# Performance work log

Hardware: AMD Instinct MI355X
Metric: run time of the kernel (lower is better)

The kernel has to match this reference:

```python
import jax, jax.numpy as jnp
import numpy as np

D_MODEL = 1024
NUM_HEADS = 16
KEY_DIM = 64
VALUE_DIM = 64
NEG_INF = jnp.float32(-1e30)


def setup_inputs() -> dict:
    key = jax.random.key(0)
    ks = jax.random.split(key, 10)
    B, S = 2, 2048
    lim = 1.0 / np.sqrt(D_MODEL)
    x = jax.random.normal(ks[0], (B, S, D_MODEL), dtype=jnp.float32)
    mask = jnp.ones((B, S), dtype=jnp.int32)  # pad mask: 1 = keep
    # stacked per-head linear params (Linear stores weight as [out, in])
    Wq = jax.random.uniform(ks[1], (NUM_HEADS, KEY_DIM, D_MODEL), jnp.float32, -lim, lim)
    bq = jax.random.uniform(ks[2], (NUM_HEADS, KEY_DIM), jnp.float32, -lim, lim)
    Wk = jax.random.uniform(ks[3], (NUM_HEADS, KEY_DIM, D_MODEL), jnp.float32, -lim, lim)
    bk = jax.random.uniform(ks[4], (NUM_HEADS, KEY_DIM), jnp.float32, -lim, lim)
    Wv = jax.random.uniform(ks[5], (NUM_HEADS, VALUE_DIM, D_MODEL), jnp.float32, -lim, lim)
    bv = jax.random.uniform(ks[6], (NUM_HEADS, VALUE_DIM), jnp.float32, -lim, lim)
    lim_o = 1.0 / np.sqrt(NUM_HEADS * VALUE_DIM)
    Wo = jax.random.uniform(ks[7], (D_MODEL, NUM_HEADS * VALUE_DIM), jnp.float32, -lim_o, lim_o)
    bo = jax.random.uniform(ks[8], (D_MODEL,), jnp.float32, -lim_o, lim_o)
    return {"x": x, "mask": mask, "Wq": Wq, "bq": bq, "Wk": Wk, "bk": bk,
            "Wv": Wv, "bv": bv, "Wo": Wo, "bo": bo}


def _mha(x, mask, Wq, bq, Wk, bk, Wv, bv, Wo, bo):
    B, S, _ = x.shape
    # per-head projections: [B, H, S, k]
    q = jnp.einsum('bsd,hkd->bhsk', x, Wq) + bq[None, :, None, :]
    k = jnp.einsum('bsd,hkd->bhsk', x, Wk) + bk[None, :, None, :]
    v = jnp.einsum('bsd,hvd->bhsv', x, Wv) + bv[None, :, None, :]
    scale = 1.0 / np.sqrt(KEY_DIM).astype(np.float32)
    scores = jnp.einsum('bhik,bhjk->bhij', q, k) * scale  # [B, H, S, S]
    # final mask = causal AND pad-row AND pad-col
    causal = jnp.tril(jnp.ones((S, S), dtype=bool))
    pad = mask.astype(bool)
    final = causal[None, None] & pad[:, None, :, None] & pad[:, None, None, :]
    masked = jnp.where(final, scores, NEG_INF)
    w = jax.nn.softmax(masked, axis=-1)
    w = jnp.where(final, w, 0.0)  # fully-masked rows -> zeros, matching loop impl
    out = jnp.einsum('bhij,bhjv->bhiv', w, v)            # [B, H, S, V]
    concat = out.transpose(0, 2, 1, 3).reshape(B, S, NUM_HEADS * VALUE_DIM)
    return concat @ Wo.T + bo


def reference(x, mask, Wq, bq, Wk, bk, Wv, bv, Wo, bo):
    return _mha(x, mask, Wq, bq, Wk, bk, Wv, bv, Wo, bo)
```

## Files before the change

kernel.cpp:

```cpp
#include <hip/hip_runtime.h>

#define SEQ 2048
#define NH 16
#define HD 64
#define DMODEL 1024

__device__ __forceinline__ unsigned int f2bf(float f) {
  unsigned int u = __float_as_uint(f);
  return ((u + 0x7fffu + ((u >> 16) & 1u)) >> 16) & 0xffffu;
}

__device__ __forceinline__ unsigned int pk2bf(float a, float b) {
  unsigned short ua = __builtin_bit_cast(unsigned short, (__bf16)a);
  unsigned short ub = __builtin_bit_cast(unsigned short, (__bf16)b);
  return (unsigned int)ua | ((unsigned int)ub << 16);
}

typedef __bf16 bf16x8 __attribute__((ext_vector_type(8)));
typedef float f32x4 __attribute__((ext_vector_type(4)));

__device__ __forceinline__ void gl2lds16(const unsigned short* g, unsigned short* l) {
  __builtin_amdgcn_global_load_lds(
      (const __attribute__((address_space(1))) unsigned int*)g,
      (__attribute__((address_space(3))) unsigned int*)l, 16, 0, 0);
}

__global__ __launch_bounds__(256) void cast_all_kernel(
    const float* __restrict__ x, const float* __restrict__ wq,
    const float* __restrict__ wk, const float* __restrict__ wv,
    const float* __restrict__ wo,
    unsigned short* __restrict__ xb, unsigned short* __restrict__ wqb,
    unsigned short* __restrict__ wkb, unsigned short* __restrict__ wvb,
    unsigned short* __restrict__ wob) {
  int idx = blockIdx.x * 256 + threadIdx.x;
  if (idx >= 1048576) return;
  const float* src;
  unsigned short* dst;
  int off;
  if (idx < 524288) {
    src = x; dst = xb; off = idx;
  } else {
    int t = idx - 524288;
    int w = t >> 17;
    off = t & 131071;
    src = (w == 0) ? wq : (w == 1) ? wk : (w == 2) ? wv : wo;
    dst = (w == 0) ? wqb : (w == 1) ? wkb : (w == 2) ? wvb : wob;
  }
  const float4* p = reinterpret_cast<const float4*>(src) + (size_t)off * 2;
  float4 a = p[0], b = p[1];
  uint4 o;
  o.x = f2bf(a.x) | (f2bf(a.y) << 16);
  o.y = f2bf(a.z) | (f2bf(a.w) << 16);
  o.z = f2bf(b.x) | (f2bf(b.y) << 16);
  o.w = f2bf(b.z) | (f2bf(b.w) << 16);
  reinterpret_cast<uint4*>(dst)[off] = o;
}

template <int MODE>
__global__ __launch_bounds__(256) void gemm128(
    const unsigned short* __restrict__ A, const unsigned short* __restrict__ B,
    const float* __restrict__ bias0, const float* __restrict__ bias1,
    const float* __restrict__ bias2, float* __restrict__ Cf,
    unsigned short* __restrict__ Qo, unsigned short* __restrict__ Ko,
    unsigned short* __restrict__ Vto, int Kdim) {
  __shared__ __align__(16) unsigned short As[128 * 64];
  __shared__ __align__(16) unsigned short Bs[128 * 64];
  const int tid = threadIdx.x;
  const int wave = tid >> 6, lane = tid & 63;
  const int wm = wave >> 1, wn = wave & 1;
  const int fr = lane & 15, quad = lane >> 4;
  const int fx = fr & 7;
  const int n0 = blockIdx.x * 128, m0 = blockIdx.y * 128;

  const int srowg = lane >> 3;
  const int schunk = (lane & 7) ^ (srowg & 7);
  const unsigned short* Abase =
      A + (size_t)(m0 + wave * 32 + srowg) * Kdim + schunk * 8;
  const unsigned short* Bbase =
      B + (size_t)(n0 + wave * 32 + srowg) * Kdim + schunk * 8;
  unsigned short* AsW = As + (wave * 32) * 64;
  unsigned short* BsW = Bs + (wave * 32) * 64;

  f32x4 acc[4][4];
#pragma unroll
  for (int mt = 0; mt < 4; ++mt)
#pragma unroll
    for (int nt = 0; nt < 4; ++nt) acc[mt][nt] = f32x4{0.f, 0.f, 0.f, 0.f};

  for (int k0 = 0; k0 < Kdim; k0 += 64) {
#pragma unroll
    for (int t = 0; t < 4; ++t) {
      gl2lds16(Abase + (size_t)(t * 8) * Kdim + k0, AsW + t * 8 * 64);
      gl2lds16(Bbase + (size_t)(t * 8) * Kdim + k0, BsW + t * 8 * 64);
    }
    __syncthreads();
#pragma unroll
    for (int ks = 0; ks < 2; ++ks) {
      bf16x8 af[4], bfv[4];
#pragma unroll
      for (int mt = 0; mt < 4; ++mt)
        af[mt] = *reinterpret_cast<const bf16x8*>(
            As + (wm * 64 + mt * 16 + fr) * 64 + ((ks * 4 + quad) ^ fx) * 8);
#pragma unroll
      for (int nt = 0; nt < 4; ++nt)
        bfv[nt] = *reinterpret_cast<const bf16x8*>(
            Bs + (wn * 64 + nt * 16 + fr) * 64 + ((ks * 4 + quad) ^ fx) * 8);
#pragma unroll
      for (int mt = 0; mt < 4; ++mt)
#pragma unroll
        for (int nt = 0; nt < 4; ++nt)
          acc[mt][nt] = __builtin_amdgcn_mfma_f32_16x16x32_bf16(
              af[mt], bfv[nt], acc[mt][nt], 0, 0, 0);
    }
    __syncthreads();
  }

  if (MODE == 0) {
    const int seg = n0 >> 10;
    const float* bp = (seg == 0) ? bias0 : (seg == 1) ? bias1 : bias2;
    const float scale = (seg == 0) ? 0.1803368809f : 1.0f;
    unsigned short* QK = (seg == 0) ? Qo : Ko;
#pragma unroll
    for (int nt = 0; nt < 4; ++nt) {
      const int c = (n0 + wn * 64 + nt * 16 + fr) & 1023;
      const int h = c >> 6, d = c & 63;
      const float bs = bp[c];
#pragma unroll
      for (int mt = 0; mt < 4; ++mt) {
        const int mbase = m0 + wm * 64 + mt * 16 + quad * 4;
        const int b = mbase >> 11, s0 = mbase & 2047;
        if (seg < 2) {
          unsigned short* dst = QK + (((size_t)(b * NH + h)) * SEQ + s0) * HD + d;
#pragma unroll
          for (int r = 0; r < 4; ++r)
            dst[(size_t)r * HD] = (unsigned short)f2bf((acc[mt][nt][r] + bs) * scale);
        } else {
          uint2 pk;
          pk.x = pk2bf(acc[mt][nt][0] + bs, acc[mt][nt][1] + bs);
          pk.y = pk2bf(acc[mt][nt][2] + bs, acc[mt][nt][3] + bs);
          *reinterpret_cast<uint2*>(
              Vto + (((size_t)(b * NH + h)) * HD + d) * SEQ + s0) = pk;
        }
      }
    }
  } else {
#pragma unroll
    for (int nt = 0; nt < 4; ++nt) {
      const int cg = n0 + wn * 64 + nt * 16 + fr;
      const float bs = bias0[cg];
#pragma unroll
      for (int mt = 0; mt < 4; ++mt) {
        const int mbase = m0 + wm * 64 + mt * 16 + quad * 4;
#pragma unroll
        for (int r = 0; r < 4; ++r)
          Cf[(size_t)(mbase + r) * DMODEL + cg] = acc[mt][nt][r] + bs;
      }
    }
  }
}

__global__ __launch_bounds__(256, 4) void attn_mfma_kernel(
    const unsigned short* __restrict__ Qg, const unsigned short* __restrict__ Kg,
    const unsigned short* __restrict__ Vtg, const int* __restrict__ mask,
    unsigned short* __restrict__ concat) {
  const int w = blockIdx.x >> 8;
  const int c = blockIdx.x & 255;
  const int gg = c >> 5;
  const int bh = c & 31;
  const int ib = (w == 0) ? (31 - gg) : (w == 1) ? gg : (w == 2) ? (23 - gg) : (8 + gg);
  const int b = bh >> 4, h = bh & 15;
  const int tid = threadIdx.x;
  const int wave = tid >> 6, lane = tid & 63;
  const int quad = lane >> 4, fr = lane & 15;
  const int fx = fr & 7;

  __shared__ __align__(16) unsigned short Ks[2][64 * 64];
  __shared__ __align__(16) unsigned short Vts[2][64 * 64];
  __shared__ __align__(16) unsigned short Pt[4][16 * 64];

  const unsigned short* Qb = Qg + ((size_t)bh * SEQ) * HD;
  const unsigned short* Kb = Kg + ((size_t)bh * SEQ) * HD;
  const unsigned short* Vtb = Vtg + ((size_t)bh * HD) * SEQ;
  const int* maskb = mask + b * SEQ;

  bool badl = false;
  {
    const int4* mp4 = reinterpret_cast<const int4*>(maskb);
#pragma unroll
    for (int u = 0; u < 8; ++u) {
      int4 v = mp4[lane * 8 + u];
      badl |= !(v.x && v.y && v.z && v.w);
    }
  }
  const unsigned long long bm = __ballot(badl);

  const int ir = ib * 64 + wave * 16 + fr;
  const bf16x8 q0 = *reinterpret_cast<const bf16x8*>(Qb + (size_t)ir * HD + quad * 8);
  const bf16x8 q1 = *reinterpret_cast<const bf16x8*>(Qb + (size_t)ir * HD + quad * 8 + 32);
  const int padi = maskb[ir];

  f32x4 o[4];
#pragma unroll
  for (int vt = 0; vt < 4; ++vt) o[vt] = f32x4{0.f, 0.f, 0.f, 0.f};
  float mr = -1e20f, lr = 0.f;

  const int srowg = lane >> 3;
  const int schunk = (lane & 7) ^ (srowg & 7);
  const unsigned short* Ksrc = Kb + (size_t)(wave * 16 + srowg) * HD + schunk * 8;
  const unsigned short* Vsrc = Vtb + (size_t)(wave * 16 + srowg) * SEQ + schunk * 8;
  const int cA0 = (quad ^ fx) * 8;
  const int cA1 = ((quad + 4) ^ fx) * 8;
  unsigned short* PtW = Pt[wave];

  {
    unsigned short* KsW = Ks[0] + (wave * 16) * 64;
    unsigned short* VtsW = Vts[0] + (wave * 16) * 64;
#pragma unroll
    for (int t = 0; t < 2; ++t) {
      gl2lds16(Ksrc + (size_t)(t * 8) * HD, KsW + t * 8 * 64);
      gl2lds16(Vsrc + (size_t)(t * 8) * SEQ, VtsW + t * 8 * 64);
    }
  }

  for (int jc = 0; jc <= ib; ++jc) {
    __syncthreads();
    if (jc < ib) {
      const int jn = (jc + 1) * 64;
      unsigned short* KsW = Ks[(jc + 1) & 1] + (wave * 16) * 64;
      unsigned short* VtsW = Vts[(jc + 1) & 1] + (wave * 16) * 64;
#pragma unroll
      for (int t = 0; t < 2; ++t) {
        gl2lds16(Ksrc + (size_t)(jn + t * 8) * HD, KsW + t * 8 * 64);
        gl2lds16(Vsrc + (size_t)(t * 8) * SEQ + jn, VtsW + t * 8 * 64);
      }
    }
    const unsigned short* Kcur = Ks[jc & 1];
    const unsigned short* Vcur = Vts[jc & 1];
    const int j0 = jc * 64;
    const bool tb = ((bm >> (2 * jc)) & 3ull) != 0ull;

    f32x4 st[4];
#pragma unroll
    for (int jt = 0; jt < 4; ++jt) {
      bf16x8 ka0 = *reinterpret_cast<const bf16x8*>(&Kcur[(jt * 16 + fr) * 64 + cA0]);
      bf16x8 ka1 = *reinterpret_cast<const bf16x8*>(&Kcur[(jt * 16 + fr) * 64 + cA1]);
      st[jt] = f32x4{0.f, 0.f, 0.f, 0.f};
      st[jt] = __builtin_amdgcn_mfma_f32_16x16x32_bf16(ka0, q0, st[jt], 0, 0, 0);
      st[jt] = __builtin_amdgcn_mfma_f32_16x16x32_bf16(ka1, q1, st[jt], 0, 0, 0);
    }

    if (tb) {
      const int4* mp = reinterpret_cast<const int4*>(maskb + j0);
#pragma unroll
      for (int jt = 0; jt < 4; ++jt) {
        const int4 mv = mp[jt * 4 + quad];
        if (mv.x == 0) st[jt][0] = -1e30f;
        if (mv.y == 0) st[jt][1] = -1e30f;
        if (mv.z == 0) st[jt][2] = -1e30f;
        if (mv.w == 0) st[jt][3] = -1e30f;
      }
    }
    if (jc == ib) {
#pragma unroll
      for (int jt = 0; jt < 4; ++jt) {
        const int jb = j0 + jt * 16 + quad * 4;
#pragma unroll
        for (int r = 0; r < 4; ++r)
          if (jb + r > ir) st[jt][r] = -1e30f;
      }
    }

    float tmax = -1e30f;
#pragma unroll
    for (int jt = 0; jt < 4; ++jt)
#pragma unroll
      for (int r = 0; r < 4; ++r) tmax = fmaxf(tmax, st[jt][r]);
    tmax = fmaxf(tmax, __shfl_xor(tmax, 16));
    tmax = fmaxf(tmax, __shfl_xor(tmax, 32));
    const bool upd = __ballot(tmax > mr) != 0ull;
    float corr = 1.f;
    if (upd) { const float mn = fmaxf(mr, tmax); corr = __builtin_amdgcn_exp2f(mr - mn); mr = mn; }
    float lloc = 0.f;
#pragma unroll
    for (int jt = 0; jt < 4; ++jt) {
      float p0 = __builtin_amdgcn_exp2f(st[jt][0] - mr);
      float p1 = __builtin_amdgcn_exp2f(st[jt][1] - mr);
      float p2 = __builtin_amdgcn_exp2f(st[jt][2] - mr);
      float p3 = __builtin_amdgcn_exp2f(st[jt][3] - mr);
      lloc += (p0 + p1) + (p2 + p3);
      uint2 pk; pk.x = pk2bf(p0, p1); pk.y = pk2bf(p2, p3);
      const int pc = (2 * jt + (quad >> 1)) ^ fx;
      *reinterpret_cast<uint2*>(&PtW[fr * 64 + pc * 8 + (quad & 1) * 4]) = pk;
    }
    lloc += __shfl_xor(lloc, 16);
    lloc += __shfl_xor(lloc, 32);
    if (upd) {
      lr = lr * corr + lloc;
#pragma unroll
      for (int vt = 0; vt < 4; ++vt) {
        o[vt][0] *= corr; o[vt][1] *= corr; o[vt][2] *= corr; o[vt][3] *= corr;
      }
    } else {
      lr += lloc;
    }

    bf16x8 pa0 = *reinterpret_cast<const bf16x8*>(&PtW[fr * 64 + (quad ^ fx) * 8]);
    bf16x8 pa1 = *reinterpret_cast<const bf16x8*>(&PtW[fr * 64 + ((quad + 4) ^ fx) * 8]);
#pragma unroll
    for (int vt = 0; vt < 4; ++vt) {
      bf16x8 vb0 = *reinterpret_cast<const bf16x8*>(&Vcur[(vt * 16 + fr) * 64 + cA0]);
      bf16x8 vb1 = *reinterpret_cast<const bf16x8*>(&Vcur[(vt * 16 + fr) * 64 + cA1]);
      o[vt] = __builtin_amdgcn_mfma_f32_16x16x32_bf16(vb0, pa0, o[vt], 0, 0, 0);
      o[vt] = __builtin_amdgcn_mfma_f32_16x16x32_bf16(vb1, pa1, o[vt], 0, 0, 0);
    }
  }

  const float inv = (padi != 0 && lr > 0.f) ? 1.f / lr : 0.f;
  unsigned short* orow = concat + ((size_t)(b * SEQ + ir)) * DMODEL + h * HD;
#pragma unroll
  for (int vt = 0; vt < 4; ++vt) {
    uint2 pk;
    pk.x = pk2bf(o[vt][0] * inv, o[vt][1] * inv);
    pk.y = pk2bf(o[vt][2] * inv, o[vt][3] * inv);
    *reinterpret_cast<uint2*>(orow + vt * 16 + quad * 4) = pk;
  }
}

extern "C" void kernel_launch(void* const* d_in, const int* in_sizes, int n_in,
                              void* d_out, int out_size, void* d_ws, size_t ws_size,
                              hipStream_t stream) {
  (void)in_sizes; (void)n_in; (void)out_size;
  const float* x  = (const float*)d_in[0];
  const int* mask = (const int*)d_in[1];
  const float* Wq = (const float*)d_in[2];
  const float* bq = (const float*)d_in[3];
  const float* Wk = (const float*)d_in[4];
  const float* bk = (const float*)d_in[5];
  const float* Wv = (const float*)d_in[6];
  const float* bv = (const float*)d_in[7];
  const float* Wo = (const float*)d_in[8];
  const float* bo = (const float*)d_in[9];
  float* out = (float*)d_out;

  char* ws = (char*)d_ws;
  if (ws_size < (48ull << 20)) return;
  unsigned short* xb  = (unsigned short*)(ws);
  unsigned short* wqb = (unsigned short*)(ws + (8ull  << 20));
  unsigned short* wkb = (unsigned short*)(ws + (10ull << 20));
  unsigned short* wvb = (unsigned short*)(ws + (12ull << 20));
  unsigned short* wob = (unsigned short*)(ws + (14ull << 20));
  unsigned short* Qb  = (unsigned short*)(ws + (16ull << 20));
  unsigned short* Kb  = (unsigned short*)(ws + (24ull << 20));
  unsigned short* Vtb = (unsigned short*)(ws + (32ull << 20));
  unsigned short* cb  = (unsigned short*)(ws + (40ull << 20));

  cast_all_kernel<<<4096, 256, 0, stream>>>(x, Wq, Wk, Wv, Wo, xb, wqb, wkb, wvb, wob);

  gemm128<0><<<dim3(24, 32), 256, 0, stream>>>(xb, wqb, bq, bk, bv,
                                               nullptr, Qb, Kb, Vtb, 1024);

  attn_mfma_kernel<<<1024, 256, 0, stream>>>(Qb, Kb, Vtb, mask, cb);

  gemm128<1><<<dim3(8, 32), 256, 0, stream>>>(cb, wob, bo, nullptr, nullptr,
                                              out, nullptr, nullptr, nullptr, 1024);
}
```

Baseline: 195.1 us.

## Keep P in registers via permuted K rows, lazy rescale, setprio, smaller output GEMM tile

The attention kernel now loads K rows into shared memory in a permuted order, so the score MFMA output layout matches the B-operand layout of the PV MFMA. P can then be packed directly in registers, which removes the per-wave Pt shared-memory round trip and its LDS writes and reads. The running max is updated lazily, only when it grows by more than 8 in log2 units. The row-sum reduction is deferred to the end of the kernel, the max reduction uses permlane32_swap, and s_setprio raises wave priority around the MFMA bursts. Separately, the output projection GEMM is templated to 64-row tiles so it launches twice as many blocks, trading per-block reuse for better CU occupancy.

```diff
diff --git a/kernel.cpp b/kernel.cpp
--- a/kernel.cpp
+++ b/kernel.cpp
@@ -18,6 +18,8 @@
 
 typedef __bf16 bf16x8 __attribute__((ext_vector_type(8)));
 typedef float f32x4 __attribute__((ext_vector_type(4)));
+typedef unsigned int uix4 __attribute__((ext_vector_type(4)));
+typedef unsigned int uix2 __attribute__((ext_vector_type(2)));
 
 __device__ __forceinline__ void gl2lds16(const unsigned short* g, unsigned short* l) {
   __builtin_amdgcn_global_load_lds(
@@ -56,57 +58,59 @@
   reinterpret_cast<uint4*>(dst)[off] = o;
 }
 
-template <int MODE>
+template <int MODE, int TM>
 __global__ __launch_bounds__(256) void gemm128(
     const unsigned short* __restrict__ A, const unsigned short* __restrict__ B,
     const float* __restrict__ bias0, const float* __restrict__ bias1,
     const float* __restrict__ bias2, float* __restrict__ Cf,
     unsigned short* __restrict__ Qo, unsigned short* __restrict__ Ko,
     unsigned short* __restrict__ Vto, int Kdim) {
-  __shared__ __align__(16) unsigned short As[128 * 64];
+  constexpr int MT = TM / 32;
+  __shared__ __align__(16) unsigned short As[TM * 64];
   __shared__ __align__(16) unsigned short Bs[128 * 64];
   const int tid = threadIdx.x;
   const int wave = tid >> 6, lane = tid & 63;
   const int wm = wave >> 1, wn = wave & 1;
   const int fr = lane & 15, quad = lane >> 4;
   const int fx = fr & 7;
-  const int n0 = blockIdx.x * 128, m0 = blockIdx.y * 128;
+  const int n0 = blockIdx.x * 128, m0 = blockIdx.y * TM;
 
   const int srowg = lane >> 3;
   const int schunk = (lane & 7) ^ (srowg & 7);
   const unsigned short* Abase =
-      A + (size_t)(m0 + wave * 32 + srowg) * Kdim + schunk * 8;
+      A + (size_t)(m0 + wave * (TM / 4) + srowg) * Kdim + schunk * 8;
   const unsigned short* Bbase =
       B + (size_t)(n0 + wave * 32 + srowg) * Kdim + schunk * 8;
-  unsigned short* AsW = As + (wave * 32) * 64;
+  unsigned short* AsW = As + (wave * (TM / 4)) * 64;
   unsigned short* BsW = Bs + (wave * 32) * 64;
 
-  f32x4 acc[4][4];
-#pragma unroll
-  for (int mt = 0; mt < 4; ++mt)
+  f32x4 acc[MT][4];
+#pragma unroll
+  for (int mt = 0; mt < MT; ++mt)
 #pragma unroll
     for (int nt = 0; nt < 4; ++nt) acc[mt][nt] = f32x4{0.f, 0.f, 0.f, 0.f};
 
   for (int k0 = 0; k0 < Kdim; k0 += 64) {
 #pragma unroll
-    for (int t = 0; t < 4; ++t) {
+    for (int t = 0; t < TM / 32; ++t)
       gl2lds16(Abase + (size_t)(t * 8) * Kdim + k0, AsW + t * 8 * 64);
+#pragma unroll
+    for (int t = 0; t < 4; ++t)
       gl2lds16(Bbase + (size_t)(t * 8) * Kdim + k0, BsW + t * 8 * 64);
-    }
     __syncthreads();
 #pragma unroll
     for (int ks = 0; ks < 2; ++ks) {
-      bf16x8 af[4], bfv[4];
-#pragma unroll
-      for (int mt = 0; mt < 4; ++mt)
+      bf16x8 af[MT], bfv[4];
+#pragma unroll
+      for (int mt = 0; mt < MT; ++mt)
         af[mt] = *reinterpret_cast<const bf16x8*>(
-            As + (wm * 64 + mt * 16 + fr) * 64 + ((ks * 4 + quad) ^ fx) * 8);
+            As + (wm * (TM / 2) + mt * 16 + fr) * 64 + ((ks * 4 + quad) ^ fx) * 8);
 #pragma unroll
       for (int nt = 0; nt < 4; ++nt)
         bfv[nt] = *reinterpret_cast<const bf16x8*>(
             Bs + (wn * 64 + nt * 16 + fr) * 64 + ((ks * 4 + quad) ^ fx) * 8);
 #pragma unroll
-      for (int mt = 0; mt < 4; ++mt)
+      for (int mt = 0; mt < MT; ++mt)
 #pragma unroll
         for (int nt = 0; nt < 4; ++nt)
           acc[mt][nt] = __builtin_amdgcn_mfma_f32_16x16x32_bf16(
@@ -126,8 +130,8 @@
       const int h = c >> 6, d = c & 63;
       const float bs = bp[c];
 #pragma unroll
-      for (int mt = 0; mt < 4; ++mt) {
-        const int mbase = m0 + wm * 64 + mt * 16 + quad * 4;
+      for (int mt = 0; mt < MT; ++mt) {
+        const int mbase = m0 + wm * (TM / 2) + mt * 16 + quad * 4;
         const int b = mbase >> 11, s0 = mbase & 2047;
         if (seg < 2) {
           unsigned short* dst = QK + (((size_t)(b * NH + h)) * SEQ + s0) * HD + d;
@@ -149,8 +153,8 @@
       const int cg = n0 + wn * 64 + nt * 16 + fr;
       const float bs = bias0[cg];
 #pragma unroll
-      for (int mt = 0; mt < 4; ++mt) {
-        const int mbase = m0 + wm * 64 + mt * 16 + quad * 4;
+      for (int mt = 0; mt < MT; ++mt) {
+        const int mbase = m0 + wm * (TM / 2) + mt * 16 + quad * 4;
 #pragma unroll
         for (int r = 0; r < 4; ++r)
           Cf[(size_t)(mbase + r) * DMODEL + cg] = acc[mt][nt][r] + bs;
@@ -176,7 +180,6 @@
 
   __shared__ __align__(16) unsigned short Ks[2][64 * 64];
   __shared__ __align__(16) unsigned short Vts[2][64 * 64];
-  __shared__ __align__(16) unsigned short Pt[4][16 * 64];
 
   const unsigned short* Qb = Qg + ((size_t)bh * SEQ) * HD;
   const unsigned short* Kb = Kg + ((size_t)bh * SEQ) * HD;
@@ -202,22 +205,23 @@
   f32x4 o[4];
 #pragma unroll
   for (int vt = 0; vt < 4; ++vt) o[vt] = f32x4{0.f, 0.f, 0.f, 0.f};
-  float mr = -1e20f, lr = 0.f;
-
-  const int srowg = lane >> 3;
-  const int schunk = (lane & 7) ^ (srowg & 7);
-  const unsigned short* Ksrc = Kb + (size_t)(wave * 16 + srowg) * HD + schunk * 8;
-  const unsigned short* Vsrc = Vtb + (size_t)(wave * 16 + srowg) * SEQ + schunk * 8;
+  float mr = -1e20f;
+  float lq = 0.f;
+
+  const int srow8 = lane >> 3;
+  const int sch8 = (lane & 7) ^ (srow8 & 7);
+  const int kprow = (wave >> 1) * 32 + ((srow8 >> 2)) * 8 + (wave & 1) * 4 + (srow8 & 3);
+  const unsigned short* Kcol = Kb + sch8 * 8;
+  const unsigned short* Vsrc = Vtb + (size_t)(wave * 16 + srow8) * SEQ + sch8 * 8;
   const int cA0 = (quad ^ fx) * 8;
   const int cA1 = ((quad + 4) ^ fx) * 8;
-  unsigned short* PtW = Pt[wave];
 
   {
     unsigned short* KsW = Ks[0] + (wave * 16) * 64;
     unsigned short* VtsW = Vts[0] + (wave * 16) * 64;
 #pragma unroll
     for (int t = 0; t < 2; ++t) {
-      gl2lds16(Ksrc + (size_t)(t * 8) * HD, KsW + t * 8 * 64);
+      gl2lds16(Kcol + (size_t)(kprow + t * 16) * HD, KsW + t * 8 * 64);
       gl2lds16(Vsrc + (size_t)(t * 8) * SEQ, VtsW + t * 8 * 64);
     }
   }
@@ -230,7 +234,7 @@
       unsigned short* VtsW = Vts[(jc + 1) & 1] + (wave * 16) * 64;
 #pragma unroll
       for (int t = 0; t < 2; ++t) {
-        gl2lds16(Ksrc + (size_t)(jn + t * 8) * HD, KsW + t * 8 * 64);
+        gl2lds16(Kcol + (size_t)(jn + kprow + t * 16) * HD, KsW + t * 8 * 64);
         gl2lds16(Vsrc + (size_t)(t * 8) * SEQ + jn, VtsW + t * 8 * 64);
       }
     }
@@ -240,6 +244,7 @@
     const bool tb = ((bm >> (2 * jc)) & 3ull) != 0ull;
 
     f32x4 st[4];
+    __builtin_amdgcn_s_setprio(1);
 #pragma unroll
     for (int jt = 0; jt < 4; ++jt) {
       bf16x8 ka0 = *reinterpret_cast<const bf16x8*>(&Kcur[(jt * 16 + fr) * 64 + cA0]);
@@ -248,12 +253,13 @@
       st[jt] = __builtin_amdgcn_mfma_f32_16x16x32_bf16(ka0, q0, st[jt], 0, 0, 0);
       st[jt] = __builtin_amdgcn_mfma_f32_16x16x32_bf16(ka1, q1, st[jt], 0, 0, 0);
     }
+    __builtin_amdgcn_s_setprio(0);
 
     if (tb) {
       const int4* mp = reinterpret_cast<const int4*>(maskb + j0);
 #pragma unroll
       for (int jt = 0; jt < 4; ++jt) {
-        const int4 mv = mp[jt * 4 + quad];
+        const int4 mv = mp[(jt >> 1) * 8 + quad * 2 + (jt & 1)];
         if (mv.x == 0) st[jt][0] = -1e30f;
         if (mv.y == 0) st[jt][1] = -1e30f;
         if (mv.z == 0) st[jt][2] = -1e30f;
@@ -263,7 +269,7 @@
     if (jc == ib) {
 #pragma unroll
       for (int jt = 0; jt < 4; ++jt) {
-        const int jb = j0 + jt * 16 + quad * 4;
+        const int jb = j0 + (jt >> 1) * 32 + quad * 8 + (jt & 1) * 4;
 #pragma unroll
         for (int r = 0; r < 4; ++r)
           if (jb + r > ir) st[jt][r] = -1e30f;
@@ -276,36 +282,37 @@
 #pragma unroll
       for (int r = 0; r < 4; ++r) tmax = fmaxf(tmax, st[jt][r]);
     tmax = fmaxf(tmax, __shfl_xor(tmax, 16));
-    tmax = fmaxf(tmax, __shfl_xor(tmax, 32));
-    const bool upd = __ballot(tmax > mr) != 0ull;
-    float corr = 1.f;
-    if (upd) { const float mn = fmaxf(mr, tmax); corr = __builtin_amdgcn_exp2f(mr - mn); mr = mn; }
-    float lloc = 0.f;
+    {
+      uix2 rr = __builtin_amdgcn_permlane32_swap(__float_as_uint(tmax),
+                                                 __float_as_uint(tmax), false, false);
+      tmax = fmaxf(__uint_as_float(rr.x), __uint_as_float(rr.y));
+    }
+    const bool upd = __ballot(tmax > mr + 8.f) != 0ull;
+    if (upd) {
+      const float mn = fmaxf(mr, tmax);
+      const float corr = __builtin_amdgcn_exp2f(mr - mn);
+      mr = mn;
+      lq *= corr;
+#pragma unroll
+      for (int vt = 0; vt < 4; ++vt) {
+        o[vt][0] *= corr; o[vt][1] *= corr; o[vt][2] *= corr; o[vt][3] *= corr;
+      }
+    }
+    unsigned int pw[8];
 #pragma unroll
     for (int jt = 0; jt < 4; ++jt) {
       float p0 = __builtin_amdgcn_exp2f(st[jt][0] - mr);
       float p1 = __builtin_amdgcn_exp2f(st[jt][1] - mr);
       float p2 = __builtin_amdgcn_exp2f(st[jt][2] - mr);
       float p3 = __builtin_amdgcn_exp2f(st[jt][3] - mr);
-      lloc += (p0 + p1) + (p2 + p3);
-      uint2 pk; pk.x = pk2bf(p0, p1); pk.y = pk2bf(p2, p3);
-      const int pc = (2 * jt + (quad >> 1)) ^ fx;
-      *reinterpret_cast<uint2*>(&PtW[fr * 64 + pc * 8 + (quad & 1) * 4]) = pk;
-    }
-    lloc += __shfl_xor(lloc, 16);
-    lloc += __shfl_xor(lloc, 32);
-    if (upd) {
-      lr = lr * corr + lloc;
-#pragma unroll
-      for (int vt = 0; vt < 4; ++vt) {
-        o[vt][0] *= corr; o[vt][1] *= corr; o[vt][2] *= corr; o[vt][3] *= corr;
-      }
-    } else {
-      lr += lloc;
-    }
-
-    bf16x8 pa0 = *reinterpret_cast<const bf16x8*>(&PtW[fr * 64 + (quad ^ fx) * 8]);
-    bf16x8 pa1 = *reinterpret_cast<const bf16x8*>(&PtW[fr * 64 + ((quad + 4) ^ fx) * 8]);
+      lq += (p0 + p1) + (p2 + p3);
+      pw[2 * jt] = pk2bf(p0, p1);
+      pw[2 * jt + 1] = pk2bf(p2, p3);
+    }
+    const bf16x8 pa0 = __builtin_bit_cast(bf16x8, uix4{pw[0], pw[1], pw[2], pw[3]});
+    const bf16x8 pa1 = __builtin_bit_cast(bf16x8, uix4{pw[4], pw[5], pw[6], pw[7]});
+
+    __builtin_amdgcn_s_setprio(1);
 #pragma unroll
     for (int vt = 0; vt < 4; ++vt) {
       bf16x8 vb0 = *reinterpret_cast<const bf16x8*>(&Vcur[(vt * 16 + fr) * 64 + cA0]);
@@ -313,8 +320,12 @@
       o[vt] = __builtin_amdgcn_mfma_f32_16x16x32_bf16(vb0, pa0, o[vt], 0, 0, 0);
       o[vt] = __builtin_amdgcn_mfma_f32_16x16x32_bf16(vb1, pa1, o[vt], 0, 0, 0);
     }
-  }
-
+    __builtin_amdgcn_s_setprio(0);
+  }
+
+  float lr = lq;
+  lr += __shfl_xor(lr, 16);
+  lr += __shfl_xor(lr, 32);
   const float inv = (padi != 0 && lr > 0.f) ? 1.f / lr : 0.f;
   unsigned short* orow = concat + ((size_t)(b * SEQ + ir)) * DMODEL + h * HD;
 #pragma unroll
@@ -356,11 +367,11 @@
 
   cast_all_kernel<<<4096, 256, 0, stream>>>(x, Wq, Wk, Wv, Wo, xb, wqb, wkb, wvb, wob);
 
-  gemm128<0><<<dim3(24, 32), 256, 0, stream>>>(xb, wqb, bq, bk, bv,
-                                               nullptr, Qb, Kb, Vtb, 1024);
+  gemm128<0, 128><<<dim3(24, 32), 256, 0, stream>>>(xb, wqb, bq, bk, bv,
+                                                    nullptr, Qb, Kb, Vtb, 1024);
 
   attn_mfma_kernel<<<1024, 256, 0, stream>>>(Qb, Kb, Vtb, mask, cb);
 
-  gemm128<1><<<dim3(8, 32), 256, 0, stream>>>(cb, wob, bo, nullptr, nullptr,
-                                              out, nullptr, nullptr, nullptr, 1024);
-}
+  gemm128<1, 64><<<dim3(8, 64), 256, 0, stream>>>(cb, wob, bo, nullptr, nullptr,
+                                                  out, nullptr, nullptr, nullptr, 1024);
+}
```

Result: faster. 186.7 us, median of 2 (-4.3%).
